# Performance work log

Hardware: AMD Instinct MI355X
Metric: run time of the kernel (lower is better)

## Reference

```python
import jax, jax.numpy as jnp
import numpy as np
from jax import lax

B, T, N, C, AD, HW, KS, KT = 32, 8, 196, 768, 192, 14, 3, 3
EPS = 1e-5

def _groupnorm1(x, gamma, beta, axes):
    # GroupNorm(1, C): normalize over channel+spatial dims per sample
    mu = jnp.mean(x, axis=axes, keepdims=True)
    var = jnp.mean((x - mu) ** 2, axis=axes, keepdims=True)
    xn = (x - mu) * lax.rsqrt(var + EPS)
    shape = [1] * x.ndim
    shape[1] = -1
    return xn * gamma.reshape(shape) + beta.reshape(shape)

def setup_inputs() -> dict:
    key = jax.random.key(0)
    ks = jax.random.split(key, 16)
    s = 0.02
    return {
        'x': jax.random.normal(ks[0], (B, T, N + 1, C), jnp.float32),
        'w_down': jax.random.normal(ks[1], (C, AD), jnp.float32) * s,
        'b_down': jnp.zeros((AD,), jnp.float32),
        'w_sdw': jax.random.normal(ks[2], (AD, 1, KS, KS), jnp.float32) * s,
        'w_spw': jax.random.normal(ks[3], (AD, AD), jnp.float32) * s,  # [out,in]
        'g_snorm': jnp.ones((AD,), jnp.float32),
        'b_snorm': jnp.zeros((AD,), jnp.float32),
        'w_diff': jax.random.normal(ks[4], (AD, AD), jnp.float32) * s,  # [in,out]
        'w_tdw': jax.random.normal(ks[5], (AD, 1, KT), jnp.float32) * s,
        'w_tpw': jax.random.normal(ks[6], (AD, AD), jnp.float32) * s,  # [out,in]
        'g_tnorm': jnp.ones((AD,), jnp.float32),
        'b_tnorm': jnp.zeros((AD,), jnp.float32),
        'w_g1': jax.random.normal(ks[7], (AD, AD), jnp.float32) * s,
        'b_g1': jnp.zeros((AD,), jnp.float32),
        'w_g2': jax.random.normal(ks[8], (AD, AD), jnp.float32) * s,
        'b_g2': jnp.zeros((AD,), jnp.float32),
        'w_up': jax.random.normal(ks[9], (AD, C), jnp.float32) * s,  # torch zero-inits; randomized for nontrivial test
        'b_up': jnp.zeros((C,), jnp.float32),
        'w_cls': jax.random.normal(ks[10], (AD, C), jnp.float32) * s,
        'b_cls': jnp.zeros((C,), jnp.float32),
    }

def reference(x, w_down, b_down, w_sdw, w_spw, g_snorm, b_snorm, w_diff,
              w_tdw, w_tpw, g_tnorm, b_tnorm, w_g1, b_g1, w_g2, b_g2,
              w_up, b_up, w_cls, b_cls):
    gelu = lambda v: jax.nn.gelu(v, approximate=False)  # torch nn.GELU default (erf)
    cls_token = x[:, :, :1, :]
    patch = x[:, :, 1:, :]
    b, t, n, _ = patch.shape
    hw = HW
    ph = patch @ w_down + b_down  # [b,t,n,ad]
    ad = ph.shape[-1]
    # spatial path: (b t) c h w
    sp = ph.reshape(b * t, hw, hw, ad).transpose(0, 3, 1, 2)
    sp = lax.conv_general_dilated(sp, w_sdw, (1, 1), 'SAME',
                                  feature_group_count=ad,
                                  dimension_numbers=('NCHW', 'OIHW', 'NCHW'))
    sp = _groupnorm1(sp, g_snorm, b_snorm, axes=(1, 2, 3))
    sp = gelu(sp)
    sp = jnp.einsum('bchw,oc->bohw', sp, w_spw)
    spatial = sp.transpose(0, 2, 3, 1).reshape(b, t, n, ad)
    # diff gating
    diff = jnp.concatenate([jnp.zeros_like(ph[:, :1]), ph[:, 1:] - ph[:, :-1]], axis=1)
    diff = diff + diff @ w_diff
    # temporal path: (b n) c t
    tp = (ph + diff).transpose(0, 2, 3, 1).reshape(b * n, ad, t)
    tp = lax.conv_general_dilated(tp, w_tdw, (1,), 'SAME',
                                  feature_group_count=ad,
                                  dimension_numbers=('NCH', 'OIH', 'NCH'))
    tp = _groupnorm1(tp, g_tnorm, b_tnorm, axes=(1, 2))
    tp = gelu(tp)
    tp = jnp.einsum('bct,oc->bot', tp, w_tpw)
    temporal = tp.reshape(b, n, ad, t).transpose(0, 3, 1, 2)
    # gate
    gi = jnp.mean(jnp.abs(diff), axis=(1, 2))  # [b, ad]
    gate = jax.nn.sigmoid(gelu(gi @ w_g1 + b_g1) @ w_g2 + b_g2)[:, None, None, :]
    fused = gate * temporal + (1.0 - gate) * spatial
    patch_out = patch + fused @ w_up + b_up
    cls_ctx = jnp.mean(fused, axis=2, keepdims=True)
    cls_out = cls_token + cls_ctx @ w_cls + b_cls
    return jnp.concatenate([cls_out, patch_out], axis=2)
```

## Files before the change

kernel.cpp:

```cpp
#include <hip/hip_runtime.h>
#include <hip/hip_bf16.h>
#include <math.h>

typedef __attribute__((ext_vector_type(8))) short s8v;
typedef __attribute__((ext_vector_type(4))) short s4v;
typedef __attribute__((ext_vector_type(4))) float f4v;

#define GN_EPS 1e-5f

__device__ __forceinline__ float s2f(short s) {
    unsigned int u = ((unsigned int)(unsigned short)s) << 16;
    float f; __builtin_memcpy(&f, &u, 4); return f;
}
__device__ __forceinline__ short f2s(float f) {
    __hip_bfloat16 h = __float2bfloat16(f);
    short s; __builtin_memcpy(&s, &h, 2); return s;
}
__device__ __forceinline__ float gelu_f(float x) {
    return 0.5f * x * (1.0f + erff(x * 0.7071067811865476f));
}
__device__ __forceinline__ void gload16(const void* g, void* l) {
    __builtin_amdgcn_global_load_lds((const __attribute__((address_space(1))) void*)g,
                                     (__attribute__((address_space(3))) void*)l,
                                     16, 0, 0);
}
template<int N> __device__ __forceinline__ void wait_vm() {
    if constexpr (N == 0) asm volatile("s_waitcnt vmcnt(0)" ::: "memory");
    else if constexpr (N == 4) asm volatile("s_waitcnt vmcnt(4)" ::: "memory");
    else if constexpr (N == 5) asm volatile("s_waitcnt vmcnt(5)" ::: "memory");
    else if constexpr (N == 6) asm volatile("s_waitcnt vmcnt(6)" ::: "memory");
    else asm volatile("s_waitcnt vmcnt(0)" ::: "memory");
}
__device__ __forceinline__ void wait_lgkm0() { asm volatile("s_waitcnt lgkmcnt(0)" ::: "memory"); }
__device__ __forceinline__ void bar() { __builtin_amdgcn_s_barrier(); }

__global__ void detect_kernel(const unsigned int* g_snorm_raw, int* flag) {
    if (threadIdx.x == 0) flag[0] = (g_snorm_raw[0] == 0x3F800000u) ? 1 : 0;
}

struct ConvArgs {
    const void* src[19];
    int cum[20];
};
__global__ __launch_bounds__(256)
void convert_kernel(ConvArgs a, short* __restrict__ dst, const int* __restrict__ dflag,
                    int total) {
    const int dt = dflag[0];
    int idx = blockIdx.x * 256 + threadIdx.x;
    const int stride = gridDim.x * 256;
    for (; idx < total; idx += stride) {
        int seg = 0;
        while (idx >= a.cum[seg + 1]) seg++;
        const int off = idx - a.cum[seg];
        const float v = dt ? ((const float*)a.src[seg])[off]
                           : s2f(((const short*)a.src[seg])[off]);
        dst[idx] = f2s(v);
    }
}

__global__ __launch_bounds__(256)
void transpose_kernel(const short* __restrict__ src, short* __restrict__ dst,
                      int R, int C) {
    const int idx = blockIdx.x * 256 + threadIdx.x;
    if (idx < R * C) {
        const int r = idx / C, c = idx - r * C;
        dst[c * R + r] = src[idx];
    }
}


#define AMAP_PLAIN 0
#define AMAP_X     1
#define AMAP_DIFF  2
#define EPI_BIASH 0
#define EPI_H     1
#define EPI_DIFF  2
#define EPI_UP    3

template<int BM, int BN, int K_DIM, int N_DIM, int AMAP, int EPI>
__global__ __launch_bounds__(256, 3)
void gemm_kernel(const void* __restrict__ Asrc, const short* __restrict__ Bmat,
                 const short* __restrict__ bias, const short* __restrict__ phH,
                 const void* __restrict__ xExt, short* __restrict__ outH,
                 void* __restrict__ outExt, float* __restrict__ giOut,
                 const int* __restrict__ dflag)
{
    constexpr int WR = BM / 2, WC = BN / 2;
    constexpr int FM = WR / 16, FN = WC / 16;
    constexpr int AL = BM / 64;
    constexpr int BL = BN / 64;
    constexpr int NK = K_DIM / 32;
    constexpr int ASZ = BM * 32, BSZ = BN * 32;
    constexpr int GL = AL + BL;
    constexpr int RL = 2 * AL + BL;

    const int dt = dflag[0];

    __shared__ short As[3 * ASZ];
    __shared__ short Bs[3 * BSZ];

    const int tid  = threadIdx.x;
    const int lane = tid & 63;
    const int wave = tid >> 6;
    const int wr = wave >> 1, wc = wave & 1;
    const int m16 = lane & 15, q = lane >> 4;
    const int rowBase = blockIdx.x * BM;
    const int colBase = blockIdx.y * BN;

    const int sr = tid >> 2;
    const int ss = tid & 3;
    const int sg = ss ^ ((sr >> 1) & 3);
    const int wOff = wave * 512;

    long aBase[AL]; int abt7[AL];
    #pragma unroll
    for (int l = 0; l < AL; l++) {
        const int grow = rowBase + sr + 64 * l;
        if constexpr (AMAP == AMAP_X) {
            const int bt = grow / 196;
            aBase[l] = (long)(grow + bt + 1) * 768 + sg * 8;
            abt7[l] = 0;
        } else if constexpr (AMAP == AMAP_DIFF) {
            aBase[l] = (long)grow * K_DIM + sg * 8;
            abt7[l] = (grow / 196) & 7;
        } else {
            aBase[l] = (long)grow * K_DIM + sg * 8;
            abt7[l] = 0;
        }
    }
    long bBase[BL];
    #pragma unroll
    for (int l = 0; l < BL; l++)
        bBase[l] = (long)(colBase + sr + 64 * l) * K_DIM + sg * 8;

    const int ra0 = wr * WR + m16;
    const int rb0 = wc * WC + m16;
    const int oA0 = ra0 * 32 + (q ^ ((ra0 >> 1) & 3)) * 8;
    const int oB0 = rb0 * 32 + (q ^ ((rb0 >> 1) & 3)) * 8;

    f4v acc[FM][FN] = {};

    auto compute = [&](int aOff, int bOff) {
        s8v af[FM], bf[FN];
        #pragma unroll
        for (int i = 0; i < FM; i++) af[i] = *(const s8v*)&As[aOff + oA0 + i * 512];
        #pragma unroll
        for (int j = 0; j < FN; j++) bf[j] = *(const s8v*)&Bs[bOff + oB0 + j * 512];
        #pragma unroll
        for (int i = 0; i < FM; i++)
            #pragma unroll
            for (int j = 0; j < FN; j++)
                acc[i][j] = __builtin_amdgcn_mfma_f32_16x16x32_bf16(bf[j], af[i], acc[i][j], 0, 0, 0);
    };
    auto gstageB = [&](int kk, int buf) {
        #pragma unroll
        for (int l = 0; l < BL; l++)
            gload16(Bmat + bBase[l] + kk, (void*)&Bs[buf * BSZ + l * 2048 + wOff]);
    };
    auto gstageA = [&](int kk, int buf) {
        #pragma unroll
        for (int l = 0; l < AL; l++)
            gload16((const short*)Asrc + aBase[l] + kk, (void*)&As[buf * ASZ + l * 2048 + wOff]);
    };

    if constexpr (AMAP == AMAP_PLAIN) {
        gstageA(0, 0);  gstageB(0, 0);
        gstageA(32, 1); gstageB(32, 1);
        wait_vm<GL>(); bar();
        int bi = 0;
        for (int t = 0; t < NK - 2; ++t) {
            int b2 = bi + 2; if (b2 >= 3) b2 -= 3;
            gstageA((t + 2) * 32, b2); gstageB((t + 2) * 32, b2);
            compute(bi * ASZ, bi * BSZ);
            wait_vm<GL>(); bar();
            bi = (bi + 1 == 3) ? 0 : bi + 1;
        }
        compute(bi * ASZ, bi * BSZ);
        wait_vm<0>(); bar();
        bi = (bi + 1 == 3) ? 0 : bi + 1;
        compute(bi * ASZ, bi * BSZ);
    } else if constexpr (AMAP == AMAP_X) {
        if (dt == 0) {
            gstageA(0, 0);  gstageB(0, 0);
            gstageA(32, 1); gstageB(32, 1);
            wait_vm<GL>(); bar();
            int bi = 0;
            for (int t = 0; t < NK - 2; ++t) {
                int b2 = bi + 2; if (b2 >= 3) b2 -= 3;
                gstageA((t + 2) * 32, b2); gstageB((t + 2) * 32, b2);
                compute(bi * ASZ, bi * BSZ);
                wait_vm<GL>(); bar();
                bi = (bi + 1 == 3) ? 0 : bi + 1;
            }
            compute(bi * ASZ, bi * BSZ);
            wait_vm<0>(); bar();
            bi = (bi + 1 == 3) ? 0 : bi + 1;
            compute(bi * ASZ, bi * BSZ);
        } else {
            f4v ra0v, ra1v, rb0v, rb1v;
            auto loadA = [&](int kk, f4v& r0, f4v& r1) {
                const float* xp = (const float*)Asrc + aBase[0] + kk;
                r0 = __builtin_nontemporal_load((const f4v*)xp);
                r1 = __builtin_nontemporal_load((const f4v*)(xp + 4));
            };
            auto writeA = [&](int idx, const f4v& r0, const f4v& r1) {
                s8v av;
                av[0] = f2s(r0.x); av[1] = f2s(r0.y); av[2] = f2s(r0.z); av[3] = f2s(r0.w);
                av[4] = f2s(r1.x); av[5] = f2s(r1.y); av[6] = f2s(r1.z); av[7] = f2s(r1.w);
                *(s8v*)&As[idx * ASZ + tid * 8] = av;
            };
            loadA(0, ra0v, ra1v); gstageB(0, 0);
            wait_vm<0>();
            writeA(0, ra0v, ra1v);
            loadA(32, ra0v, ra1v); gstageB(32, 1);
            wait_lgkm0(); bar();
            int bi = 0;
            for (int t = 0; t < NK - 2; ++t) {
                int b2 = bi + 2; if (b2 >= 3) b2 -= 3;
                loadA((t + 2) * 32, rb0v, rb1v); gstageB((t + 2) * 32, b2);
                compute((t & 1) * ASZ, bi * BSZ);
                wait_vm<RL>();
                writeA((t + 1) & 1, ra0v, ra1v);
                wait_lgkm0(); bar();
                ra0v = rb0v; ra1v = rb1v;
                bi = (bi + 1 == 3) ? 0 : bi + 1;
            }
            compute(((NK - 2) & 1) * ASZ, bi * BSZ);
            wait_vm<0>();
            writeA((NK - 1) & 1, ra0v, ra1v);
            wait_lgkm0(); bar();
            bi = (bi + 1 == 3) ? 0 : bi + 1;
            compute(((NK - 1) & 1) * ASZ, bi * BSZ);
        }
    } else {
        s8v ra1v, ra0v, rb1v, rb0v;
        auto loadA = [&](int kk, s8v& v1, s8v& v0) {
            const short* p1 = (const short*)Asrc + aBase[0] + kk;
            const short* p0 = p1 - (abt7[0] ? 37632 : 0);
            v1 = *(const s8v*)p1;
            v0 = *(const s8v*)p0;
        };
        auto writeA = [&](int idx, const s8v& v1, const s8v& v0) {
            s8v av;
            if (abt7[0]) {
                #pragma unroll
                for (int j = 0; j < 8; j++) av[j] = f2s(s2f(v1[j]) - s2f(v0[j]));
            } else {
                #pragma unroll
                for (int j = 0; j < 8; j++) av[j] = 0;
            }
            *(s8v*)&As[idx * ASZ + tid * 8] = av;
        };
        loadA(0, ra1v, ra0v); gstageB(0, 0);
        wait_vm<0>();
        writeA(0, ra1v, ra0v);
        loadA(32, ra1v, ra0v); gstageB(32, 1);
        wait_lgkm0(); bar();
        int bi = 0;
        for (int t = 0; t < NK - 2; ++t) {
            int b2 = bi + 2; if (b2 >= 3) b2 -= 3;
            loadA((t + 2) * 32, rb1v, rb0v); gstageB((t + 2) * 32, b2);
            compute((t & 1) * ASZ, bi * BSZ);
            wait_vm<RL>();
            writeA((t + 1) & 1, ra1v, ra0v);
            wait_lgkm0(); bar();
            ra1v = rb1v; ra0v = rb0v;
            bi = (bi + 1 == 3) ? 0 : bi + 1;
        }
        compute(((NK - 2) & 1) * ASZ, bi * BSZ);
        wait_vm<0>();
        writeA((NK - 1) & 1, ra1v, ra0v);
        wait_lgkm0(); bar();
        bi = (bi + 1 == 3) ? 0 : bi + 1;
        compute(((NK - 1) & 1) * ASZ, bi * BSZ);
    }

    #pragma unroll
    for (int fi = 0; fi < FM; fi++) {
        const int grow = rowBase + wr * WR + fi * 16 + m16;
        const int gcb  = colBase + wc * WC + q * 4;

        if constexpr (EPI == EPI_BIASH) {
            #pragma unroll
            for (int fj = 0; fj < FN; fj++) {
                const int gc = gcb + fj * 16;
                const s4v bv = *(const s4v*)&bias[gc];
                s4v o;
                #pragma unroll
                for (int r = 0; r < 4; r++) o[r] = f2s(acc[fi][fj][r] + s2f(bv[r]));
                *(s4v*)&outH[(long)grow * N_DIM + gc] = o;
            }
        } else if constexpr (EPI == EPI_H) {
            #pragma unroll
            for (int fj = 0; fj < FN; fj++) {
                const int gc = gcb + fj * 16;
                s4v o;
                #pragma unroll
                for (int r = 0; r < 4; r++) o[r] = f2s(acc[fi][fj][r]);
                *(s4v*)&outH[(long)grow * N_DIM + gc] = o;
            }
        } else if constexpr (EPI == EPI_DIFF) {
            const int t = (grow / 196) & 7;
            float ga[FN * 4];
            #pragma unroll
            for (int fj = 0; fj < FN; fj++) {
                const int gc = gcb + fj * 16;
                const long pOff = (long)grow * 192 + gc;
                const s4v p1 = *(const s4v*)&phH[pOff];
                s4v p0 = p1;
                if (t > 0) p0 = *(const s4v*)&phH[pOff - 37632];
                s4v o;
                #pragma unroll
                for (int r = 0; r < 4; r++) {
                    const float phv = s2f(p1[r]);
                    const float d = (t > 0) ? (phv - s2f(p0[r])) : 0.0f;
                    const float tpmp = acc[fi][fj][r] + d;
                    ga[fj * 4 + r] = fabsf(tpmp);
                    o[r] = f2s(tpmp + phv);
                }
                *(s4v*)&outH[pOff] = o;
            }
            #pragma unroll
            for (int mlt = 1; mlt < 16; mlt <<= 1) {
                #pragma unroll
                for (int k = 0; k < FN * 4; k++) ga[k] += __shfl_xor(ga[k], mlt, 64);
            }
            if (m16 == 0) {
                const int b = (rowBase + wr * WR + fi * 16) / 1568;
                #pragma unroll
                for (int k = 0; k < FN * 4; k++) {
                    const int col = colBase + wc * WC + (k >> 2) * 16 + q * 4 + (k & 3);
                    atomicAdd(&giOut[b * 192 + col], ga[k]);
                }
            }
        } else {
            const int bt = grow / 196;
            const long orow = (long)(grow + bt + 1) * 768;
            #pragma unroll
            for (int fj = 0; fj < FN; fj++) {
                const int gc = gcb + fj * 16;
                const s4v bv = *(const s4v*)&bias[gc];
                if (dt) {
                    const f4v xv = __builtin_nontemporal_load(
                        (const f4v*)((const float*)xExt + orow + gc));
                    f4v ov;
                    ov.x = xv.x + acc[fi][fj][0] + s2f(bv[0]);
                    ov.y = xv.y + acc[fi][fj][1] + s2f(bv[1]);
                    ov.z = xv.z + acc[fi][fj][2] + s2f(bv[2]);
                    ov.w = xv.w + acc[fi][fj][3] + s2f(bv[3]);
                    __builtin_nontemporal_store(ov, (f4v*)((float*)outExt + orow + gc));
                } else {
                    const s4v xv = *(const s4v*)((const short*)xExt + orow + gc);
                    s4v ov;
                    #pragma unroll
                    for (int r = 0; r < 4; r++)
                        ov[r] = f2s(s2f(xv[r]) + acc[fi][fj][r] + s2f(bv[r]));
                    *(s4v*)((short*)outExt + orow + gc) = ov;
                }
            }
        }
    }
}

__global__ __launch_bounds__(1024, 4)
void spatial_kernel(const short* __restrict__ ph, const short* __restrict__ w_sdw,
                    const short* __restrict__ g_s, const short* __restrict__ b_s,
                    short* __restrict__ snorm)
{
    __shared__ short tile[196 * 192];
    __shared__ short wkT[9 * 192];
    __shared__ float gsl[192], bsl[192];
    __shared__ float redA[16], redB[16];
    __shared__ float stats[2];

    const int bt = blockIdx.x, tid = threadIdx.x;
    const short* Pg = ph + (long)bt * 37632;

    for (int i = tid; i < 4704; i += 1024)
        *(s8v*)&tile[i * 8] = *(const s8v*)&Pg[i * 8];
    for (int i = tid; i < 1728; i += 1024) {
        const int c = i / 9, tap = i - c * 9;
        wkT[tap * 192 + c] = w_sdw[i];
    }
    if (tid < 192) { gsl[tid] = s2f(g_s[tid]); bsl[tid] = s2f(b_s[tid]); }
    __syncthreads();

    float val[5][8];
    float lsum = 0.f, lsq = 0.f;
    #pragma unroll
    for (int it = 0; it < 5; it++) {
        const int i = tid + it * 1024;
        #pragma unroll
        for (int k = 0; k < 8; k++) val[it][k] = 0.f;
        if (i < 4704) {
            const int n = i / 24, c8 = i - n * 24;
            const int h = n / 14, w = n - (n / 14) * 14;
            float a[8] = {0.f,0.f,0.f,0.f,0.f,0.f,0.f,0.f};
            #pragma unroll
            for (int tap = 0; tap < 9; tap++) {
                const int dh = tap / 3 - 1, dw = tap % 3 - 1;
                const int hh = h + dh, ww = w + dw;
                if (hh >= 0 && hh < 14 && ww >= 0 && ww < 14) {
                    s8v iv = *(const s8v*)&tile[(hh * 14 + ww) * 192 + c8 * 8];
                    s8v wv = *(const s8v*)&wkT[tap * 192 + c8 * 8];
                    #pragma unroll
                    for (int k = 0; k < 8; k++) a[k] += s2f(iv[k]) * s2f(wv[k]);
                }
            }
            #pragma unroll
            for (int k = 0; k < 8; k++) {
                val[it][k] = a[k]; lsum += a[k]; lsq += a[k] * a[k];
            }
        }
    }
    #pragma unroll
    for (int d = 1; d < 64; d <<= 1) {
        lsum += __shfl_xor(lsum, d, 64);
        lsq  += __shfl_xor(lsq,  d, 64);
    }
    if ((tid & 63) == 0) { redA[tid >> 6] = lsum; redB[tid >> 6] = lsq; }
    __syncthreads();
    if (tid < 64) {
        float s = (tid < 16) ? redA[tid] : 0.f;
        float qq = (tid < 16) ? redB[tid] : 0.f;
        #pragma unroll
        for (int d = 1; d < 16; d <<= 1) {
            s  += __shfl_xor(s,  d, 64);
            qq += __shfl_xor(qq, d, 64);
        }
        if (tid == 0) {
            const float inv = 1.0f / 37632.0f;
            const float mean = s * inv;
            const float var  = qq * inv - mean * mean;
            stats[0] = mean; stats[1] = rsqrtf(var + GN_EPS);
        }
    }
    __syncthreads();
    const float mean = stats[0], rstd = stats[1];
    short* Og = snorm + (long)bt * 37632;
    #pragma unroll
    for (int it = 0; it < 5; it++) {
        const int i = tid + it * 1024;
        if (i < 4704) {
            const int c8 = i - (i / 24) * 24;
            s8v o;
            #pragma unroll
            for (int k = 0; k < 8; k++) {
                const int c = c8 * 8 + k;
                const float y = (val[it][k] - mean) * rstd * gsl[c] + bsl[c];
                o[k] = f2s(gelu_f(y));
            }
            *(s8v*)&Og[i * 8] = o;
        }
    }
}

__global__ __launch_bounds__(192)
void temporal_kernel(const short* __restrict__ tp, const short* __restrict__ w_tdw,
                     const short* __restrict__ g_t, const short* __restrict__ b_t,
                     short* __restrict__ tnorm)
{
    const int bn = blockIdx.x;
    const int c = threadIdx.x;
    const int b = bn / 196, n = bn - (bn / 196) * 196;
    const long base = ((long)b * 8 * 196 + n) * 192 + c;
    const long ts = 196 * 192;
    float v[8], o[8];
    #pragma unroll
    for (int t = 0; t < 8; t++) v[t] = s2f(tp[base + t * ts]);
    const float w0 = s2f(w_tdw[c * 3]), w1 = s2f(w_tdw[c * 3 + 1]), w2 = s2f(w_tdw[c * 3 + 2]);
    #pragma unroll
    for (int t = 0; t < 8; t++) {
        float a = v[t] * w1;
        if (t > 0) a += v[t - 1] * w0;
        if (t < 7) a += v[t + 1] * w2;
        o[t] = a;
    }
    float lsum = 0.f, lsq = 0.f;
    #pragma unroll
    for (int t = 0; t < 8; t++) { lsum += o[t]; lsq += o[t] * o[t]; }
    __shared__ float red1[192], red2[192];
    red1[c] = lsum; red2[c] = lsq;
    __syncthreads();
    for (int s = 96; s > 2; s >>= 1) {
        if (c < s) { red1[c] += red1[c + s]; red2[c] += red2[c + s]; }
        __syncthreads();
    }
    const float mean = (red1[0] + red1[1] + red1[2]) * (1.0f / 1536.0f);
    const float var  = (red2[0] + red2[1] + red2[2]) * (1.0f / 1536.0f) - mean * mean;
    const float rstd = rsqrtf(var + GN_EPS);
    const float gg = s2f(g_t[c]), bb = s2f(b_t[c]);
    #pragma unroll
    for (int t = 0; t < 8; t++) {
        const float y = (o[t] - mean) * rstd * gg + bb;
        tnorm[base + t * ts] = f2s(gelu_f(y));
    }
}

__global__ __launch_bounds__(192)
void gate_kernel(const float* __restrict__ gi, const short* __restrict__ w_g1,
                 const short* __restrict__ b_g1, const short* __restrict__ w_g2,
                 const short* __restrict__ b_g2, float* __restrict__ gate)
{
    const int b = blockIdx.x, o = threadIdx.x;
    __shared__ float s0[192], s1[192];
    s0[o] = gi[b * 192 + o] * (1.0f / 1568.0f);
    __syncthreads();
    float a = s2f(b_g1[o]);
    for (int cc = 0; cc < 192; cc++) a += s0[cc] * s2f(w_g1[cc * 192 + o]);
    s1[o] = gelu_f(a);
    __syncthreads();
    float a2 = s2f(b_g2[o]);
    for (int cc = 0; cc < 192; cc++) a2 += s1[cc] * s2f(w_g2[cc * 192 + o]);
    gate[b * 192 + o] = 1.0f / (1.0f + expf(-a2));
}

__global__ __launch_bounds__(192)
void fuse_kernel(const short* __restrict__ temporal, const short* __restrict__ spatial,
                 const float* __restrict__ gate, short* __restrict__ fused,
                 float* __restrict__ cls_sum)
{
    const int bt = blockIdx.x;
    const int b = bt >> 3;
    const int tid = threadIdx.x;
    const int c8 = tid >> 3, sub = tid & 7;
    float g[8];
    {
        const f4v* gp = (const f4v*)&gate[b * 192 + c8 * 8];
        f4v ga = gp[0], gb = gp[1];
        g[0]=ga.x; g[1]=ga.y; g[2]=ga.z; g[3]=ga.w;
        g[4]=gb.x; g[5]=gb.y; g[6]=gb.z; g[7]=gb.w;
    }
    float part[8] = {0.f,0.f,0.f,0.f,0.f,0.f,0.f,0.f};
    for (int n = sub; n < 196; n += 8) {
        const long off = ((long)bt * 196 + n) * 192 + c8 * 8;
        s8v tv = *(const s8v*)(temporal + off);
        s8v sv = *(const s8v*)(spatial + off);
        s8v fv;
        #pragma unroll
        for (int k = 0; k < 8; k++) {
            const float f = g[k] * s2f(tv[k]) + (1.0f - g[k]) * s2f(sv[k]);
            fv[k] = f2s(f);
            part[k] += f;
        }
        *(s8v*)(fused + off) = fv;
    }
    #pragma unroll
    for (int d = 1; d < 8; d <<= 1) {
        #pragma unroll
        for (int k = 0; k < 8; k++) part[k] += __shfl_xor(part[k], d, 64);
    }
    if (sub == 0) {
        #pragma unroll
        for (int k = 0; k < 8; k++)
            cls_sum[bt * 192 + c8 * 8 + k] = part[k] * (1.0f / 196.0f);
    }
}

__global__ __launch_bounds__(256)
void cls_kernel(const float* __restrict__ cls_sum, const short* __restrict__ w_cls,
                const short* __restrict__ b_cls, const void* __restrict__ x,
                void* __restrict__ out, const int* __restrict__ dflag)
{
    const int dt = dflag[0];
    const int bt = blockIdx.x, tid = threadIdx.x;
    __shared__ float ctx[192];
    if (tid < 192) ctx[tid] = cls_sum[bt * 192 + tid];
    __syncthreads();
    for (int oc = tid; oc < 768; oc += 256) {
        float a = s2f(b_cls[oc]);
        for (int cc = 0; cc < 192; cc++) a += ctx[cc] * s2f(w_cls[cc * 768 + oc]);
        const long oi = (long)bt * 197 * 768 + oc;
        if (dt) ((float*)out)[oi] = ((const float*)x)[oi] + a;
        else    ((short*)out)[oi] = f2s(s2f(((const short*)x)[oi]) + a);
    }
}

extern "C" void kernel_launch(void* const* d_in, const int* in_sizes, int n_in,
                              void* d_out, int out_size, void* d_ws, size_t ws_size,
                              hipStream_t stream) {
    const void* x = d_in[0];

    const long F = 50176L * 192L;
    short* wsS = (short*)d_ws;
    short* P = wsS;
    short* Q = wsS + F;
    short* R = wsS + 2 * F;
    short* S = wsS + 3 * F;
    short* W = wsS + 4 * F;
    int cum[20]; cum[0] = 0;
    for (int i = 1; i <= 19; i++) cum[i] = cum[i - 1] + in_sizes[i];
    const int totalW = cum[19];

    short* WT   = W + ((totalW + 7) & ~7);
    short* wdT  = WT;
    short* wdfT = WT + 147456;
    short* wupT = WT + 147456 + 36864;

    float* smalls = (float*)(WT + 331776);
    float* gi      = smalls;
    float* gate    = smalls + 6144;
    float* cls_sum = smalls + 12288;
    int*   dflag   = (int*)(smalls + 61440);

    const short* b_down = W + cum[1];
    const short* w_sdw  = W + cum[2];
    const short* w_spw  = W + cum[3];
    const short* g_sn   = W + cum[4];
    const short* b_sn   = W + cum[5];
    const short* w_tdw  = W + cum[7];
    const short* w_tpw  = W + cum[8];
    const short* g_tn   = W + cum[9];
    const short* b_tn   = W + cum[10];
    const short* w_g1   = W + cum[11];
    const short* b_g1   = W + cum[12];
    const short* w_g2   = W + cum[13];
    const short* b_g2   = W + cum[14];
    const short* b_up   = W + cum[16];
    const short* w_cls  = W + cum[17];
    const short* b_cls  = W + cum[18];

    hipMemsetAsync(gi, 0, 6144 * sizeof(float), stream);
    detect_kernel<<<1, 64, 0, stream>>>((const unsigned int*)d_in[5], dflag);

    ConvArgs ca;
    for (int i = 0; i < 19; i++) ca.src[i] = d_in[i + 1];
    for (int i = 0; i < 20; i++) ca.cum[i] = cum[i];
    convert_kernel<<<618, 256, 0, stream>>>(ca, W, dflag, totalW);

    transpose_kernel<<<576, 256, 0, stream>>>(W + cum[0],  wdT,  768, 192);
    transpose_kernel<<<144, 256, 0, stream>>>(W + cum[6],  wdfT, 192, 192);
    transpose_kernel<<<576, 256, 0, stream>>>(W + cum[15], wupT, 192, 768);

    gemm_kernel<64, 192, 768, 192, AMAP_X, EPI_BIASH>
        <<<dim3(784, 1), 256, 0, stream>>>(x, wdT, b_down, nullptr, nullptr, P, nullptr, nullptr, dflag);
    spatial_kernel<<<256, 1024, 0, stream>>>(P, w_sdw, g_sn, b_sn, R);
    gemm_kernel<64, 192, 192, 192, AMAP_PLAIN, EPI_H>
        <<<dim3(784, 1), 256, 0, stream>>>(R, w_spw, nullptr, nullptr, nullptr, S, nullptr, nullptr, dflag);
    gemm_kernel<64, 192, 192, 192, AMAP_DIFF, EPI_DIFF>
        <<<dim3(784, 1), 256, 0, stream>>>(P, wdfT, nullptr, P, nullptr, Q, nullptr, gi, dflag);
    temporal_kernel<<<6272, 192, 0, stream>>>(Q, w_tdw, g_tn, b_tn, R);
    gemm_kernel<64, 192, 192, 192, AMAP_PLAIN, EPI_H>
        <<<dim3(784, 1), 256, 0, stream>>>(R, w_tpw, nullptr, nullptr, nullptr, Q, nullptr, nullptr, dflag);
    gate_kernel<<<32, 192, 0, stream>>>(gi, w_g1, b_g1, w_g2, b_g2, gate);
    fuse_kernel<<<256, 192, 0, stream>>>(Q, S, gate, R, cls_sum);
    gemm_kernel<128, 128, 192, 768, AMAP_PLAIN, EPI_UP>
        <<<dim3(392, 6), 256, 0, stream>>>(R, wupT, b_up, nullptr, x, nullptr, d_out, nullptr, dflag);
    cls_kernel<<<256, 256, 0, stream>>>(cls_sum, w_cls, b_cls, x, d_out, dflag);
}
```

Measured before the change: 615.7 us.

## Switch all GEMMs to 64x64 tiles with XCD-aware block swizzle

Every GEMM now uses a fixed 64x64 tile instead of 64x192 or 128x128, and the 2D grid becomes a 1D grid remapped so consecutive blocks are spread across the 8 XCDs. Launch bounds rise to 6 blocks per CU. The up-projection epilogue swaps the MFMA operands, so each lane writes scalar elements along columns in the transposed layout instead of 4-wide vectors. The goal is more parallelism and occupancy plus better L2 locality. The cost is less reuse per tile, with A re-read three or twelve times, and narrower stores in the largest output write.

```diff
diff --git a/kernel.cpp b/kernel.cpp
--- a/kernel.cpp
+++ b/kernel.cpp
@@ -26,10 +26,14 @@
 }
 template<int N> __device__ __forceinline__ void wait_vm() {
     if constexpr (N == 0) asm volatile("s_waitcnt vmcnt(0)" ::: "memory");
+    else if constexpr (N == 1) asm volatile("s_waitcnt vmcnt(1)" ::: "memory");
+    else if constexpr (N == 2) asm volatile("s_waitcnt vmcnt(2)" ::: "memory");
+    else if constexpr (N == 3) asm volatile("s_waitcnt vmcnt(3)" ::: "memory");
     else if constexpr (N == 4) asm volatile("s_waitcnt vmcnt(4)" ::: "memory");
     else if constexpr (N == 5) asm volatile("s_waitcnt vmcnt(5)" ::: "memory");
     else if constexpr (N == 6) asm volatile("s_waitcnt vmcnt(6)" ::: "memory");
-    else asm volatile("s_waitcnt vmcnt(0)" ::: "memory");
+    else if constexpr (N == 7) asm volatile("s_waitcnt vmcnt(7)" ::: "memory");
+    else asm volatile("s_waitcnt vmcnt(8)" ::: "memory");
 }
 __device__ __forceinline__ void wait_lgkm0() { asm volatile("s_waitcnt lgkmcnt(0)" ::: "memory"); }
 __device__ __forceinline__ void bar() { __builtin_amdgcn_s_barrier(); }
@@ -77,22 +81,20 @@
 #define EPI_DIFF  2
 #define EPI_UP    3
 
-template<int BM, int BN, int K_DIM, int N_DIM, int AMAP, int EPI>
-__global__ __launch_bounds__(256, 3)
+template<int K_DIM, int N_DIM, int GY, int AMAP, int EPI, bool SWAP>
+__global__ __launch_bounds__(256, 6)
 void gemm_kernel(const void* __restrict__ Asrc, const short* __restrict__ Bmat,
                  const short* __restrict__ bias, const short* __restrict__ phH,
                  const void* __restrict__ xExt, short* __restrict__ outH,
                  void* __restrict__ outExt, float* __restrict__ giOut,
                  const int* __restrict__ dflag)
 {
-    constexpr int WR = BM / 2, WC = BN / 2;
-    constexpr int FM = WR / 16, FN = WC / 16;
-    constexpr int AL = BM / 64;
-    constexpr int BL = BN / 64;
     constexpr int NK = K_DIM / 32;
-    constexpr int ASZ = BM * 32, BSZ = BN * 32;
-    constexpr int GL = AL + BL;
-    constexpr int RL = 2 * AL + BL;
+    constexpr int ASZ = 64 * 32, BSZ = 64 * 32;
+    constexpr int GL = 2;
+    constexpr int RL = 3;
+    constexpr int NBLK = 784 * GY;
+    constexpr int CPX = NBLK / 8;
 
     const int dt = dflag[0];
 
@@ -104,63 +106,59 @@
     const int wave = tid >> 6;
     const int wr = wave >> 1, wc = wave & 1;
     const int m16 = lane & 15, q = lane >> 4;
-    const int rowBase = blockIdx.x * BM;
-    const int colBase = blockIdx.y * BN;
+
+    const int lin = blockIdx.x;
+    const int swz = (lin & 7) * CPX + (lin >> 3);
+    const int bx = swz / GY, by = swz - bx * GY;
+    const int rowBase = bx * 64;
+    const int colBase = by * 64;
 
     const int sr = tid >> 2;
     const int ss = tid & 3;
     const int sg = ss ^ ((sr >> 1) & 3);
     const int wOff = wave * 512;
 
-    long aBase[AL]; int abt7[AL];
-    #pragma unroll
-    for (int l = 0; l < AL; l++) {
-        const int grow = rowBase + sr + 64 * l;
-        if constexpr (AMAP == AMAP_X) {
-            const int bt = grow / 196;
-            aBase[l] = (long)(grow + bt + 1) * 768 + sg * 8;
-            abt7[l] = 0;
-        } else if constexpr (AMAP == AMAP_DIFF) {
-            aBase[l] = (long)grow * K_DIM + sg * 8;
-            abt7[l] = (grow / 196) & 7;
-        } else {
-            aBase[l] = (long)grow * K_DIM + sg * 8;
-            abt7[l] = 0;
-        }
-    }
-    long bBase[BL];
-    #pragma unroll
-    for (int l = 0; l < BL; l++)
-        bBase[l] = (long)(colBase + sr + 64 * l) * K_DIM + sg * 8;
-
-    const int ra0 = wr * WR + m16;
-    const int rb0 = wc * WC + m16;
+    const int agrow = rowBase + sr;
+    long aBase; int abt7 = 0;
+    if constexpr (AMAP == AMAP_X) {
+        const int bt = agrow / 196;
+        aBase = (long)(agrow + bt + 1) * 768 + sg * 8;
+    } else if constexpr (AMAP == AMAP_DIFF) {
+        aBase = (long)agrow * K_DIM + sg * 8;
+        abt7 = (agrow / 196) & 7;
+    } else {
+        aBase = (long)agrow * K_DIM + sg * 8;
+    }
+    const long bBase = (long)(colBase + sr) * K_DIM + sg * 8;
+
+    const int ra0 = wr * 32 + m16;
+    const int rb0 = wc * 32 + m16;
     const int oA0 = ra0 * 32 + (q ^ ((ra0 >> 1) & 3)) * 8;
     const int oB0 = rb0 * 32 + (q ^ ((rb0 >> 1) & 3)) * 8;
 
-    f4v acc[FM][FN] = {};
+    f4v acc[2][2] = {};
 
     auto compute = [&](int aOff, int bOff) {
-        s8v af[FM], bf[FN];
-        #pragma unroll
-        for (int i = 0; i < FM; i++) af[i] = *(const s8v*)&As[aOff + oA0 + i * 512];
-        #pragma unroll
-        for (int j = 0; j < FN; j++) bf[j] = *(const s8v*)&Bs[bOff + oB0 + j * 512];
-        #pragma unroll
-        for (int i = 0; i < FM; i++)
+        s8v af[2], bf[2];
+        #pragma unroll
+        for (int i = 0; i < 2; i++) af[i] = *(const s8v*)&As[aOff + oA0 + i * 512];
+        #pragma unroll
+        for (int j = 0; j < 2; j++) bf[j] = *(const s8v*)&Bs[bOff + oB0 + j * 512];
+        #pragma unroll
+        for (int i = 0; i < 2; i++)
             #pragma unroll
-            for (int j = 0; j < FN; j++)
-                acc[i][j] = __builtin_amdgcn_mfma_f32_16x16x32_bf16(bf[j], af[i], acc[i][j], 0, 0, 0);
+            for (int j = 0; j < 2; j++) {
+                if constexpr (SWAP)
+                    acc[i][j] = __builtin_amdgcn_mfma_f32_16x16x32_bf16(bf[j], af[i], acc[i][j], 0, 0, 0);
+                else
+                    acc[i][j] = __builtin_amdgcn_mfma_f32_16x16x32_bf16(af[i], bf[j], acc[i][j], 0, 0, 0);
+            }
     };
     auto gstageB = [&](int kk, int buf) {
-        #pragma unroll
-        for (int l = 0; l < BL; l++)
-            gload16(Bmat + bBase[l] + kk, (void*)&Bs[buf * BSZ + l * 2048 + wOff]);
+        gload16(Bmat + bBase + kk, (void*)&Bs[buf * BSZ + wOff]);
     };
     auto gstageA = [&](int kk, int buf) {
-        #pragma unroll
-        for (int l = 0; l < AL; l++)
-            gload16((const short*)Asrc + aBase[l] + kk, (void*)&As[buf * ASZ + l * 2048 + wOff]);
+        gload16((const short*)Asrc + aBase + kk, (void*)&As[buf * ASZ + wOff]);
     };
 
     if constexpr (AMAP == AMAP_PLAIN) {
@@ -199,7 +197,7 @@
         } else {
             f4v ra0v, ra1v, rb0v, rb1v;
             auto loadA = [&](int kk, f4v& r0, f4v& r1) {
-                const float* xp = (const float*)Asrc + aBase[0] + kk;
+                const float* xp = (const float*)Asrc + aBase + kk;
                 r0 = __builtin_nontemporal_load((const f4v*)xp);
                 r1 = __builtin_nontemporal_load((const f4v*)(xp + 4));
             };
@@ -235,14 +233,14 @@
     } else {
         s8v ra1v, ra0v, rb1v, rb0v;
         auto loadA = [&](int kk, s8v& v1, s8v& v0) {
-            const short* p1 = (const short*)Asrc + aBase[0] + kk;
-            const short* p0 = p1 - (abt7[0] ? 37632 : 0);
+            const short* p1 = (const short*)Asrc + aBase + kk;
+            const short* p0 = p1 - (abt7 ? 37632 : 0);
             v1 = *(const s8v*)p1;
             v0 = *(const s8v*)p0;
         };
         auto writeA = [&](int idx, const s8v& v1, const s8v& v0) {
             s8v av;
-            if (abt7[0]) {
+            if (abt7) {
                 #pragma unroll
                 for (int j = 0; j < 8; j++) av[j] = f2s(s2f(v1[j]) - s2f(v0[j]));
             } else {
@@ -275,87 +273,86 @@
         compute(((NK - 1) & 1) * ASZ, bi * BSZ);
     }
 
-    #pragma unroll
-    for (int fi = 0; fi < FM; fi++) {
-        const int grow = rowBase + wr * WR + fi * 16 + m16;
-        const int gcb  = colBase + wc * WC + q * 4;
-
-        if constexpr (EPI == EPI_BIASH) {
+    if constexpr (SWAP) {
+        #pragma unroll
+        for (int fi = 0; fi < 2; fi++) {
+            const int grow = rowBase + wr * 32 + fi * 16 + m16;
+            const int gcb  = colBase + wc * 32 + q * 4;
+
+            if constexpr (EPI == EPI_BIASH) {
+                #pragma unroll
+                for (int fj = 0; fj < 2; fj++) {
+                    const int gc = gcb + fj * 16;
+                    const s4v bv = *(const s4v*)&bias[gc];
+                    s4v o;
+                    #pragma unroll
+                    for (int r = 0; r < 4; r++) o[r] = f2s(acc[fi][fj][r] + s2f(bv[r]));
+                    *(s4v*)&outH[(long)grow * N_DIM + gc] = o;
+                }
+            } else if constexpr (EPI == EPI_H) {
+                #pragma unroll
+                for (int fj = 0; fj < 2; fj++) {
+                    const int gc = gcb + fj * 16;
+                    s4v o;
+                    #pragma unroll
+                    for (int r = 0; r < 4; r++) o[r] = f2s(acc[fi][fj][r]);
+                    *(s4v*)&outH[(long)grow * N_DIM + gc] = o;
+                }
+            } else if constexpr (EPI == EPI_DIFF) {
+                const int t = (grow / 196) & 7;
+                float ga[8];
+                #pragma unroll
+                for (int fj = 0; fj < 2; fj++) {
+                    const int gc = gcb + fj * 16;
+                    const long pOff = (long)grow * 192 + gc;
+                    const s4v p1 = *(const s4v*)&phH[pOff];
+                    s4v p0 = p1;
+                    if (t > 0) p0 = *(const s4v*)&phH[pOff - 37632];
+                    s4v o;
+                    #pragma unroll
+                    for (int r = 0; r < 4; r++) {
+                        const float phv = s2f(p1[r]);
+                        const float d = (t > 0) ? (phv - s2f(p0[r])) : 0.0f;
+                        const float tpmp = acc[fi][fj][r] + d;
+                        ga[fj * 4 + r] = fabsf(tpmp);
+                        o[r] = f2s(tpmp + phv);
+                    }
+                    *(s4v*)&outH[pOff] = o;
+                }
+                #pragma unroll
+                for (int mlt = 1; mlt < 16; mlt <<= 1) {
+                    #pragma unroll
+                    for (int k = 0; k < 8; k++) ga[k] += __shfl_xor(ga[k], mlt, 64);
+                }
+                if (m16 == 0) {
+                    const int b = (rowBase + wr * 32 + fi * 16) / 1568;
+                    #pragma unroll
+                    for (int k = 0; k < 8; k++) {
+                        const int col = colBase + wc * 32 + (k >> 2) * 16 + q * 4 + (k & 3);
+                        atomicAdd(&giOut[b * 192 + col], ga[k]);
+                    }
+                }
+            }
+        }
+    } else {
+        #pragma unroll
+        for (int fi = 0; fi < 2; fi++) {
             #pragma unroll
-            for (int fj = 0; fj < FN; fj++) {
-                const int gc = gcb + fj * 16;
-                const s4v bv = *(const s4v*)&bias[gc];
-                s4v o;
+            for (int r = 0; r < 4; r++) {
+                const int grow = rowBase + wr * 32 + fi * 16 + q * 4 + r;
+                const int bt = grow / 196;
+                const long orow = (long)(grow + bt + 1) * 768;
                 #pragma unroll
-                for (int r = 0; r < 4; r++) o[r] = f2s(acc[fi][fj][r] + s2f(bv[r]));
-                *(s4v*)&outH[(long)grow * N_DIM + gc] = o;
-            }
-        } else if constexpr (EPI == EPI_H) {
-            #pragma unroll
-            for (int fj = 0; fj < FN; fj++) {
-                const int gc = gcb + fj * 16;
-                s4v o;
-                #pragma unroll
-                for (int r = 0; r < 4; r++) o[r] = f2s(acc[fi][fj][r]);
-                *(s4v*)&outH[(long)grow * N_DIM + gc] = o;
-            }
-        } else if constexpr (EPI == EPI_DIFF) {
-            const int t = (grow / 196) & 7;
-            float ga[FN * 4];
-            #pragma unroll
-            for (int fj = 0; fj < FN; fj++) {
-                const int gc = gcb + fj * 16;
-                const long pOff = (long)grow * 192 + gc;
-                const s4v p1 = *(const s4v*)&phH[pOff];
-                s4v p0 = p1;
-                if (t > 0) p0 = *(const s4v*)&phH[pOff - 37632];
-                s4v o;
-                #pragma unroll
-                for (int r = 0; r < 4; r++) {
-                    const float phv = s2f(p1[r]);
-                    const float d = (t > 0) ? (phv - s2f(p0[r])) : 0.0f;
-                    const float tpmp = acc[fi][fj][r] + d;
-                    ga[fj * 4 + r] = fabsf(tpmp);
-                    o[r] = f2s(tpmp + phv);
-                }
-                *(s4v*)&outH[pOff] = o;
-            }
-            #pragma unroll
-            for (int mlt = 1; mlt < 16; mlt <<= 1) {
-                #pragma unroll
-                for (int k = 0; k < FN * 4; k++) ga[k] += __shfl_xor(ga[k], mlt, 64);
-            }
-            if (m16 == 0) {
-                const int b = (rowBase + wr * WR + fi * 16) / 1568;
-                #pragma unroll
-                for (int k = 0; k < FN * 4; k++) {
-                    const int col = colBase + wc * WC + (k >> 2) * 16 + q * 4 + (k & 3);
-                    atomicAdd(&giOut[b * 192 + col], ga[k]);
-                }
-            }
-        } else {
-            const int bt = grow / 196;
-            const long orow = (long)(grow + bt + 1) * 768;
-            #pragma unroll
-            for (int fj = 0; fj < FN; fj++) {
-                const int gc = gcb + fj * 16;
-                const s4v bv = *(const s4v*)&bias[gc];
-                if (dt) {
-                    const f4v xv = __builtin_nontemporal_load(
-                        (const f4v*)((const float*)xExt + orow + gc));
-                    f4v ov;
-                    ov.x = xv.x + acc[fi][fj][0] + s2f(bv[0]);
-                    ov.y = xv.y + acc[fi][fj][1] + s2f(bv[1]);
-                    ov.z = xv.z + acc[fi][fj][2] + s2f(bv[2]);
-                    ov.w = xv.w + acc[fi][fj][3] + s2f(bv[3]);
-                    __builtin_nontemporal_store(ov, (f4v*)((float*)outExt + orow + gc));
-                } else {
-                    const s4v xv = *(const s4v*)((const short*)xExt + orow + gc);
-                    s4v ov;
-                    #pragma unroll
-                    for (int r = 0; r < 4; r++)
-                        ov[r] = f2s(s2f(xv[r]) + acc[fi][fj][r] + s2f(bv[r]));
-                    *(s4v*)((short*)outExt + orow + gc) = ov;
+                for (int fj = 0; fj < 2; fj++) {
+                    const int gc = colBase + wc * 32 + fj * 16 + m16;
+                    const float bv = s2f(bias[gc]);
+                    const float v = acc[fi][fj][r] + bv;
+                    if (dt) {
+                        ((float*)outExt)[orow + gc] = ((const float*)xExt)[orow + gc] + v;
+                    } else {
+                        ((short*)outExt)[orow + gc] =
+                            f2s(s2f(((const short*)xExt)[orow + gc]) + v);
+                    }
                 }
             }
         }
@@ -632,19 +629,19 @@
     transpose_kernel<<<144, 256, 0, stream>>>(W + cum[6],  wdfT, 192, 192);
     transpose_kernel<<<576, 256, 0, stream>>>(W + cum[15], wupT, 192, 768);
 
-    gemm_kernel<64, 192, 768, 192, AMAP_X, EPI_BIASH>
-        <<<dim3(784, 1), 256, 0, stream>>>(x, wdT, b_down, nullptr, nullptr, P, nullptr, nullptr, dflag);
+    gemm_kernel<768, 192, 3, AMAP_X, EPI_BIASH, true>
+        <<<784 * 3, 256, 0, stream>>>(x, wdT, b_down, nullptr, nullptr, P, nullptr, nullptr, dflag);
     spatial_kernel<<<256, 1024, 0, stream>>>(P, w_sdw, g_sn, b_sn, R);
-    gemm_kernel<64, 192, 192, 192, AMAP_PLAIN, EPI_H>
-        <<<dim3(784, 1), 256, 0, stream>>>(R, w_spw, nullptr, nullptr, nullptr, S, nullptr, nullptr, dflag);
-    gemm_kernel<64, 192, 192, 192, AMAP_DIFF, EPI_DIFF>
-        <<<dim3(784, 1), 256, 0, stream>>>(P, wdfT, nullptr, P, nullptr, Q, nullptr, gi, dflag);
+    gemm_kernel<192, 192, 3, AMAP_PLAIN, EPI_H, true>
+        <<<784 * 3, 256, 0, stream>>>(R, w_spw, nullptr, nullptr, nullptr, S, nullptr, nullptr, dflag);
+    gemm_kernel<192, 192, 3, AMAP_DIFF, EPI_DIFF, true>
+        <<<784 * 3, 256, 0, stream>>>(P, wdfT, nullptr, P, nullptr, Q, nullptr, gi, dflag);
     temporal_kernel<<<6272, 192, 0, stream>>>(Q, w_tdw, g_tn, b_tn, R);
-    gemm_kernel<64, 192, 192, 192, AMAP_PLAIN, EPI_H>
-        <<<dim3(784, 1), 256, 0, stream>>>(R, w_tpw, nullptr, nullptr, nullptr, Q, nullptr, nullptr, dflag);
+    gemm_kernel<192, 192, 3, AMAP_PLAIN, EPI_H, true>
+        <<<784 * 3, 256, 0, stream>>>(R, w_tpw, nullptr, nullptr, nullptr, Q, nullptr, nullptr, dflag);
     gate_kernel<<<32, 192, 0, stream>>>(gi, w_g1, b_g1, w_g2, b_g2, gate);
     fuse_kernel<<<256, 192, 0, stream>>>(Q, S, gate, R, cls_sum);
-    gemm_kernel<128, 128, 192, 768, AMAP_PLAIN, EPI_UP>
-        <<<dim3(392, 6), 256, 0, stream>>>(R, wupT, b_up, nullptr, x, nullptr, d_out, nullptr, dflag);
+    gemm_kernel<192, 768, 12, AMAP_PLAIN, EPI_UP, false>
+        <<<784 * 12, 256, 0, stream>>>(R, wupT, b_up, nullptr, x, nullptr, d_out, nullptr, dflag);
     cls_kernel<<<256, 256, 0, stream>>>(cls_sum, w_cls, b_cls, x, d_out, dflag);
 }
```

After: 645.0 us. 1.05x slower.
